# Performance work log

Hardware: AMD Instinct MI355X
Metric: run time of the kernel (lower is better)

## Reference

```python
import jax, jax.numpy as jnp
import numpy as np

TEMP = 1.0  # composition softmax temperature

def _bank_topk(x, U, V, logits, top_k):
    # softmax over primitive logits, select top-k, renormalize, fused low-rank projection
    w = jax.nn.softmax(logits / TEMP)                     # [P]
    tw, ti = jax.lax.top_k(w, top_k)                      # [k], [k]
    tw = tw / tw.sum()
    Us = U[ti]                                            # [k, d_in, r]
    Vs = V[ti]                                            # [k, r, d_out]
    h = jnp.einsum('bsd,kdr->bksr', x, Us)                # low-rank bottleneck
    return jnp.einsum('bksr,kro,k->bso', h, Vs, tw)       # weighted fuse

def reference(x, q_U, q_V, k_U, k_V, v_U, v_V, q_logits, k_logits, v_logits, out_w, top_k):
    B, S, _ = x.shape
    H, D = 16, 64
    q = _bank_topk(x, q_U, q_V, q_logits, top_k)
    k = _bank_topk(x, k_U, k_V, k_logits, top_k)
    v = _bank_topk(x, v_U, v_V, v_logits, top_k)
    q = q.reshape(B, S, H, D).transpose(0, 2, 1, 3)       # [B,H,S,D]
    k = k.reshape(B, S, H, D).transpose(0, 2, 1, 3)
    v = v.reshape(B, S, H, D).transpose(0, 2, 1, 3)
    scale = 1.0 / jnp.sqrt(jnp.asarray(D, dtype=x.dtype))
    scores = jnp.einsum('bhqd,bhkd->bhqk', q, k) * scale  # [B,H,S,S]
    causal = jnp.triu(jnp.ones((S, S), dtype=bool), 1)
    scores = jnp.where(causal[None, None], jnp.finfo(x.dtype).min, scores)
    probs = jax.nn.softmax(scores, axis=-1)
    out = jnp.einsum('bhqk,bhkd->bhqd', probs, v)
    out = out.transpose(0, 2, 1, 3).reshape(B, S, H * D)
    return out @ out_w.T                                   # nn.Linear(H*D, d_model, bias=False)

def setup_inputs() -> dict:
    key = jax.random.key(0)
    ks = jax.random.split(key, 11)
    P, d, r = 16, 1024, 64
    B, S = 4, 1024
    f = jnp.float32
    inp = {
        'x': jax.random.normal(ks[0], (B, S, d), f),
        'q_U': jax.random.normal(ks[1], (P, d, r), f) * (1.0 / np.sqrt(d)),
        'q_V': jax.random.normal(ks[2], (P, r, d), f) * (1.0 / np.sqrt(r)),
        'k_U': jax.random.normal(ks[3], (P, d, r), f) * (1.0 / np.sqrt(d)),
        'k_V': jax.random.normal(ks[4], (P, r, d), f) * (1.0 / np.sqrt(r)),
        'v_U': jax.random.normal(ks[5], (P, d, r), f) * (1.0 / np.sqrt(d)),
        'v_V': jax.random.normal(ks[6], (P, r, d), f) * (1.0 / np.sqrt(r)),
        'q_logits': jax.random.normal(ks[7], (P,), f) * 0.01,
        'k_logits': jax.random.normal(ks[8], (P,), f) * 0.01,
        'v_logits': jax.random.normal(ks[9], (P,), f) * 0.01,
        'out_w': jax.random.normal(ks[10], (d, d), f) * (1.0 / np.sqrt(d)),
        'top_k': 4,
    }
    return inp
```

## Files before the change

### kernel.cpp

```cpp
#include <hip/hip_runtime.h>
#include <math.h>

#define D_MODEL 1024
#define RANK    64
#define PMAX    16
#define S_LEN   1024
#define HD      64
#define MROWS   4096
#define NHEAD   16
#define BATCH   4

typedef short short8v __attribute__((ext_vector_type(8)));
typedef float floatx4 __attribute__((ext_vector_type(4)));

typedef __attribute__((address_space(1))) const unsigned int* gptr_t;
typedef __attribute__((address_space(3))) unsigned int* lptr_t;

static __device__ __forceinline__ void async16(const void* g, void* l) {
    __builtin_amdgcn_global_load_lds((gptr_t)g, (lptr_t)l, 16, 0, 0);
}

static __device__ __forceinline__ short f2bf(float f) {
    unsigned int u = __float_as_uint(f);
    u = (u + 0x7fffu + ((u >> 16) & 1u)) >> 16;
    return (short)u;
}

static __device__ __forceinline__ void topk_select(
    const float* __restrict__ lg, int K, int j, int* p_out, float* w_out) {
    float l[PMAX];
#pragma unroll
    for (int i = 0; i < PMAX; ++i) l[i] = lg[i];
    bool used[PMAX];
#pragma unroll
    for (int i = 0; i < PMAX; ++i) used[i] = false;
    float first = 0.f, sum = 0.f, sl = 0.f;
    int sel = 0;
    for (int jj = 0; jj < K; ++jj) {
        int best = -1; float bv = -INFINITY;
        for (int i = 0; i < PMAX; ++i)
            if (!used[i] && l[i] > bv) { bv = l[i]; best = i; }
        used[best] = true;
        if (jj == 0) first = bv;
        float e = __expf(bv - first);
        sum += e;
        if (jj == j) { sel = best; sl = e; }
    }
    if (j < K) { *p_out = sel; *w_out = sl / sum; }
    else       { *p_out = 0;   *w_out = 0.f; }
}

__global__ __launch_bounds__(256) void prep_all_kernel(
    const float* __restrict__ x,
    const float* __restrict__ qU, const float* __restrict__ kU,
    const float* __restrict__ vU,
    const float* __restrict__ qV, const float* __restrict__ kV,
    const float* __restrict__ vV,
    const float* __restrict__ qlg, const float* __restrict__ klg,
    const float* __restrict__ vlg,
    const int* __restrict__ topk, const float* __restrict__ outw,
    short* __restrict__ xb, short* __restrict__ wb,
    short* __restrict__ Ut, short* __restrict__ Vt) {
    int b = blockIdx.x;
    int t = threadIdx.x;
    if (b < 4096) {
        int i = b * 256 + t;
        float4 f = ((const float4*)x)[i];
        short4 o;
        o.x = f2bf(f.x); o.y = f2bf(f.y); o.z = f2bf(f.z); o.w = f2bf(f.w);
        ((short4*)xb)[i] = o;
        return;
    }
    if (b < 5120) {
        int i = (b - 4096) * 256 + t;
        float4 f = ((const float4*)outw)[i];
        short4 o;
        o.x = f2bf(f.x); o.y = f2bf(f.y); o.z = f2bf(f.z); o.w = f2bf(f.w);
        ((short4*)wb)[i] = o;
        return;
    }
    int rem  = b - 5120;
    int z    = rem >> 8;
    int j    = (rem >> 4) & 15;
    int tile = rem & 15;
    int bank = (z < 3) ? z : z - 3;
    int K = *topk; if (K < 1) K = 1; if (K > PMAX) K = PMAX;
    const float* lg = (bank == 0) ? qlg : (bank == 1) ? klg : vlg;
    int p; float wj;
    topk_select(lg, K, j, &p, &wj);

    __shared__ float T[64][65];
    if (z < 3) {
        const float* U = (bank == 0) ? qU : (bank == 1) ? kU : vU;
        const float* src = U + (size_t)p * D_MODEL * RANK;
        int d0 = tile * 64;
        int rl = t & 63, dq = t >> 6;
#pragma unroll
        for (int i = 0; i < 16; ++i) {
            int dl = i * 4 + dq;
            T[rl][dl] = src[(size_t)(d0 + dl) * RANK + rl];
        }
        __syncthreads();
        short* dst = Ut + (size_t)bank * D_MODEL * D_MODEL;
        int rr = t >> 2;
#pragma unroll
        for (int i = 0; i < 4; ++i) {
            int c = (t & 3) * 16 + i * 4;
            short4 o;
            o.x = f2bf(T[rr][c + 0]); o.y = f2bf(T[rr][c + 1]);
            o.z = f2bf(T[rr][c + 2]); o.w = f2bf(T[rr][c + 3]);
            *(short4*)&dst[(size_t)(j * 64 + rr) * D_MODEL + d0 + c] = o;
        }
    } else {
        const float* V = (bank == 0) ? qV : (bank == 1) ? kV : vV;
        const float* src = V + (size_t)p * RANK * D_MODEL;
        int n0 = tile * 64;
        int nl = t & 63, rq = t >> 6;
#pragma unroll
        for (int i = 0; i < 16; ++i) {
            int rl = i * 4 + rq;
            T[nl][rl] = src[(size_t)rl * D_MODEL + n0 + nl] * wj;
        }
        __syncthreads();
        short* dst = Vt + (size_t)bank * D_MODEL * D_MODEL;
        int rr = t >> 2;
#pragma unroll
        for (int i = 0; i < 4; ++i) {
            int c = (t & 3) * 16 + i * 4;
            short4 o;
            o.x = f2bf(T[rr][c + 0]); o.y = f2bf(T[rr][c + 1]);
            o.z = f2bf(T[rr][c + 2]); o.w = f2bf(T[rr][c + 3]);
            *(short4*)&dst[(size_t)(n0 + rr) * D_MODEL + j * 64 + c] = o;
        }
    }
}

static __device__ __forceinline__ void gemm_stage(
    const short* __restrict__ A, const short* __restrict__ B,
    int m0, int n0, int k0, short* Ab, short* Bb,
    int w, int srow, int skoff) {
    async16(A + (size_t)(m0 + w * 16 + srow) * D_MODEL + k0 + skoff,
            Ab + (w * 16 + srow) * 32 + skoff);
    async16(A + (size_t)(m0 + 64 + w * 16 + srow) * D_MODEL + k0 + skoff,
            Ab + (64 + w * 16 + srow) * 32 + skoff);
    async16(B + (size_t)(n0 + w * 16 + srow) * D_MODEL + k0 + skoff,
            Bb + (w * 16 + srow) * 32 + skoff);
    async16(B + (size_t)(n0 + 64 + w * 16 + srow) * D_MODEL + k0 + skoff,
            Bb + (64 + w * 16 + srow) * 32 + skoff);
}

static __device__ __forceinline__ void mfma_gemm_tile(
    const short* __restrict__ A, const short* __restrict__ B, int kl,
    int m0, int n0, short* As, short* Bs, floatx4 acc[4][4]) {
    const int t    = threadIdx.x;
    const int w    = t >> 6;
    const int lane = t & 63;
    const int wm   = w & 1, wn = w >> 1;
    const int colL = lane & 15, quad = lane >> 4;
    const int srow  = lane >> 2;
    const int skoff = (lane & 3) * 8;

#pragma unroll
    for (int i = 0; i < 4; ++i)
#pragma unroll
        for (int j = 0; j < 4; ++j) acc[i][j] = (floatx4){0.f, 0.f, 0.f, 0.f};

    gemm_stage(A, B, m0, n0, 0, As, Bs, w, srow, skoff);
    __syncthreads();
    const int nk = kl >> 5;
    int cur = 0;
    for (int kt = 0; kt < nk; ++kt) {
        if (kt + 1 < nk)
            gemm_stage(A, B, m0, n0, (kt + 1) * 32,
                       As + ((cur ^ 1) << 12), Bs + ((cur ^ 1) << 12),
                       w, srow, skoff);
        const short* Ab = As + (cur << 12);
        const short* Bb = Bs + (cur << 12);
        short8v af[4], bf[4];
#pragma unroll
        for (int i = 0; i < 4; ++i)
            af[i] = *(const short8v*)&Ab[(wm * 64 + i * 16 + colL) * 32 + quad * 8];
#pragma unroll
        for (int j = 0; j < 4; ++j)
            bf[j] = *(const short8v*)&Bb[(wn * 64 + j * 16 + colL) * 32 + quad * 8];
#pragma unroll
        for (int i = 0; i < 4; ++i)
#pragma unroll
            for (int j = 0; j < 4; ++j)
                acc[i][j] = __builtin_amdgcn_mfma_f32_16x16x32_bf16(af[i], bf[j], acc[i][j], 0, 0, 0);
        __syncthreads();
        cur ^= 1;
    }
}

__global__ __launch_bounds__(256) void gemm_h_kernel(
    const short* __restrict__ xb, const short* __restrict__ Ut,
    const int* __restrict__ topk, short* __restrict__ h) {
    int K = *topk; if (K < 1) K = 1; if (K > PMAX) K = PMAX;
    int n0 = blockIdx.y * 128;
    if (n0 >= K * 64) return;
    int m0 = blockIdx.x * 128;
    int bank = blockIdx.z;
    __shared__ short As[8192];
    __shared__ short Bs[8192];
    floatx4 acc[4][4];
    mfma_gemm_tile(xb, Ut + (size_t)bank * D_MODEL * D_MODEL, D_MODEL, m0, n0, As, Bs, acc);

    const int t = threadIdx.x, w = t >> 6, lane = t & 63;
    const int wm = w & 1, wn = w >> 1, colL = lane & 15, quad = lane >> 4;
    short* H = h + (size_t)bank * MROWS * D_MODEL;
#pragma unroll
    for (int i = 0; i < 4; ++i)
#pragma unroll
        for (int j = 0; j < 4; ++j)
#pragma unroll
            for (int r = 0; r < 4; ++r)
                H[(size_t)(m0 + wm * 64 + i * 16 + quad * 4 + r) * D_MODEL +
                  (n0 + wn * 64 + j * 16 + colL)] = f2bf(acc[i][j][r]);
}

__global__ __launch_bounds__(256) void gemm_qkv_kernel(
    const short* __restrict__ h, const short* __restrict__ Vt,
    const int* __restrict__ topk, short* __restrict__ qkv) {
    int K = *topk; if (K < 1) K = 1; if (K > PMAX) K = PMAX;
    int m0 = blockIdx.x * 128;
    int n0 = blockIdx.y * 128;
    int bank = blockIdx.z;
    __shared__ short As[8192];
    __shared__ short Bs[8192];
    floatx4 acc[4][4];
    mfma_gemm_tile(h + (size_t)bank * MROWS * D_MODEL,
                   Vt + (size_t)bank * D_MODEL * D_MODEL, K * 64, m0, n0, As, Bs, acc);

    const int t = threadIdx.x, w = t >> 6, lane = t & 63;
    const int wm = w & 1, wn = w >> 1, colL = lane & 15, quad = lane >> 4;
    short* outp = qkv + (size_t)bank * MROWS * D_MODEL;
    const float scl = (bank == 0) ? 0.18033688f : 1.0f;
#pragma unroll
    for (int i = 0; i < 4; ++i)
#pragma unroll
        for (int j = 0; j < 4; ++j)
#pragma unroll
            for (int r = 0; r < 4; ++r) {
                int m = m0 + wm * 64 + i * 16 + quad * 4 + r;
                int n = n0 + wn * 64 + j * 16 + colL;
                int b = m >> 10, s = m & 1023;
                int head = n >> 6, d = n & 63;
                outp[(((size_t)(b * NHEAD + head) << 10) + s) * HD + d] = f2bf(acc[i][j][r] * scl);
            }
}

__global__ __launch_bounds__(256) void transpose_v_kernel(
    const short* __restrict__ src, short* __restrict__ dst) {
    int st = blockIdx.x, bh = blockIdx.y;
    __shared__ short T[64][72];
    const short* S = src + (size_t)bh * (S_LEN * HD) + (size_t)st * 64 * HD;
    int r = threadIdx.x >> 2, i = threadIdx.x & 3;
    *(short8v*)&T[r][i * 16]     = *(const short8v*)&S[r * HD + i * 16];
    *(short8v*)&T[r][i * 16 + 8] = *(const short8v*)&S[r * HD + i * 16 + 8];
    __syncthreads();
    short* Drow = dst + (size_t)bh * (S_LEN * HD) + (size_t)r * S_LEN + st * 64 + i * 16;
    short8v o0, o1;
#pragma unroll
    for (int k = 0; k < 8; ++k) o0[k] = T[i * 16 + k][r];
#pragma unroll
    for (int k = 0; k < 8; ++k) o1[k] = T[i * 16 + 8 + k][r];
    *(short8v*)&Drow[0] = o0;
    *(short8v*)&Drow[8] = o1;
}

static __device__ __forceinline__ void attn_stage(
    const short* __restrict__ Kg, const short* __restrict__ Vg, int base,
    short* KsB, short* VsB, int w, int lane) {
#pragma unroll
    for (int q2 = 0; q2 < 4; ++q2) {
        int row = w * 32 + q2 * 8 + (lane >> 3);
        int i   = lane & 7;
        int g   = i ^ (row & 7);
        async16(Kg + (size_t)(base + row) * HD + g * 8, KsB + row * 64 + i * 8);
    }
#pragma unroll
    for (int q2 = 0; q2 < 4; ++q2) {
        int d    = w * 16 + q2 * 4 + (lane >> 4);
        int i    = lane & 15;
        int half = i >> 3, i3 = i & 7;
        int g3   = i3 ^ (d & 7);
        async16(Vg + (size_t)d * S_LEN + base + half * 64 + g3 * 8,
                VsB + d * 128 + i * 8);
    }
}

template<int NN, bool DIAG>
static __device__ __forceinline__ void attn_step(
    const short* KsB, const short* VsB, short* Pw,
    short8v aq0, short8v aq1, int w, int col, int quad,
    floatx4& O0, floatx4& O1, floatx4& O2, floatx4& O3,
    float mrow[4], float lrow[4]) {
    const int cl7 = col & 7;
    float sc[NN][4];
#pragma unroll
    for (int n = 0; n < NN; ++n) {
        const int dn = n - (NN - 4);
        if (DIAG && dn > w) {
#pragma unroll
            for (int r = 0; r < 4; ++r) sc[n][r] = -INFINITY;
        } else {
            floatx4 z = {0.f, 0.f, 0.f, 0.f};
            const short* kb = KsB + (n * 16 + col) * 64;
            short8v b0 = *(const short8v*)(kb + ((quad ^ cl7) << 3));
            short8v b1 = *(const short8v*)(kb + (((quad + 4) ^ cl7) << 3));
            z = __builtin_amdgcn_mfma_f32_16x16x32_bf16(aq0, b0, z, 0, 0, 0);
            z = __builtin_amdgcn_mfma_f32_16x16x32_bf16(aq1, b1, z, 0, 0, 0);
            if (DIAG && dn == w) {
#pragma unroll
                for (int r = 0; r < 4; ++r)
                    if (col > quad * 4 + r) z[r] = -INFINITY;
            }
#pragma unroll
            for (int r = 0; r < 4; ++r) sc[n][r] = z[r];
        }
    }
    float pv[NN][4];
#pragma unroll
    for (int r = 0; r < 4; ++r) {
        float tm = sc[0][r];
#pragma unroll
        for (int n = 1; n < NN; ++n) tm = fmaxf(tm, sc[n][r]);
        tm = fmaxf(tm, __shfl_xor(tm, 1));
        tm = fmaxf(tm, __shfl_xor(tm, 2));
        tm = fmaxf(tm, __shfl_xor(tm, 4));
        tm = fmaxf(tm, __shfl_xor(tm, 8));
        float mnew  = fmaxf(mrow[r], tm);
        float alpha = exp2f(mrow[r] - mnew);
        float ps = 0.f;
#pragma unroll
        for (int n = 0; n < NN; ++n) {
            float p = exp2f(sc[n][r] - mnew);
            pv[n][r] = p;
            ps += p;
        }
        lrow[r] = lrow[r] * alpha + ps;
        mrow[r] = mnew;
        O0[r] *= alpha; O1[r] *= alpha; O2[r] *= alpha; O3[r] *= alpha;
    }
#pragma unroll
    for (int h = 0; h < NN / 4; ++h) {
#pragma unroll
        for (int n2 = 0; n2 < 4; ++n2)
#pragma unroll
            for (int r = 0; r < 4; ++r)
                Pw[(quad * 4 + r) * 72 + n2 * 16 + col] = f2bf(pv[h * 4 + n2][r]);
        const int kslim = DIAG ? ((NN - 4 + w) >> 1) : 3;
#pragma unroll
        for (int ks2 = 2 * h; ks2 < 2 * h + 2; ++ks2) {
            if (DIAG && ks2 > kslim) break;
            short8v ap = *(const short8v*)(Pw + col * 72 + (ks2 & 1) * 32 + quad * 8);
            const int half = ks2 >> 1;
            const int i3   = (ks2 & 1) * 4 + quad;
            const int swz  = ((i3 ^ cl7) << 3);
            const short* vb = VsB + half * 64 + swz;
            short8v v0 = *(const short8v*)(vb + (0  + col) * 128);
            short8v v1 = *(const short8v*)(vb + (16 + col) * 128);
            short8v v2 = *(const short8v*)(vb + (32 + col) * 128);
            short8v v3 = *(const short8v*)(vb + (48 + col) * 128);
            O0 = __builtin_amdgcn_mfma_f32_16x16x32_bf16(ap, v0, O0, 0, 0, 0);
            O1 = __builtin_amdgcn_mfma_f32_16x16x32_bf16(ap, v1, O1, 0, 0, 0);
            O2 = __builtin_amdgcn_mfma_f32_16x16x32_bf16(ap, v2, O2, 0, 0, 0);
            O3 = __builtin_amdgcn_mfma_f32_16x16x32_bf16(ap, v3, O3, 0, 0, 0);
        }
    }
}

__global__ __launch_bounds__(256) void attn_mfma_kernel(
    const short* __restrict__ qkv,
    const short* __restrict__ vtb,
    short* __restrict__ attn_out) {
    const int t    = threadIdx.x;
    const int w    = t >> 6;
    const int lane = t & 63;
    const int col  = lane & 15;
    const int quad = lane >> 4;
    const int pr   = blockIdx.x;
    const int bh   = blockIdx.y;
    const size_t HS   = (size_t)S_LEN * HD;
    const size_t BSTR = (size_t)MROWS * D_MODEL;
    const short* Qg = qkv + (size_t)bh * HS;
    const short* Kg = qkv + BSTR + (size_t)bh * HS;
    const short* Vg = vtb + (size_t)bh * HS;

    __shared__ short Ks[2][8192];
    __shared__ short Vs[2][8192];
    __shared__ short Ps[4][1152];
    short* Pw = Ps[w];

    for (int ph = 0; ph < 2; ++ph) {
        const int qt = ph ? (15 - pr) : pr;
        const int qrow = qt * 64 + w * 16 + col;
        short8v aq0 = *(const short8v*)(Qg + (size_t)qrow * HD + quad * 8);
        short8v aq1 = *(const short8v*)(Qg + (size_t)qrow * HD + 32 + quad * 8);
        floatx4 O0 = {0.f, 0.f, 0.f, 0.f}, O1 = O0, O2 = O0, O3 = O0;
        float mrow[4] = {-INFINITY, -INFINITY, -INFINITY, -INFINITY};
        float lrow[4] = {0.f, 0.f, 0.f, 0.f};

        const int nC = (qt + 2) >> 1;
        __syncthreads();
        attn_stage(Kg, Vg, 0, Ks[0], Vs[0], w, lane);
        __syncthreads();
        int cur = 0;
        for (int c = 0; c + 1 < nC; ++c) {
            attn_stage(Kg, Vg, (c + 1) * 128, Ks[cur ^ 1], Vs[cur ^ 1], w, lane);
            attn_step<8, false>(Ks[cur], Vs[cur], Pw, aq0, aq1, w, col, quad,
                                O0, O1, O2, O3, mrow, lrow);
            __syncthreads();
            cur ^= 1;
        }
        if (qt & 1)
            attn_step<8, true>(Ks[cur], Vs[cur], Pw, aq0, aq1, w, col, quad,
                               O0, O1, O2, O3, mrow, lrow);
        else
            attn_step<4, true>(Ks[cur], Vs[cur], Pw, aq0, aq1, w, col, quad,
                               O0, O1, O2, O3, mrow, lrow);

        const int b  = bh >> 4;
        const int hh = bh & 15;
        short* orow = attn_out +
            ((size_t)(b * S_LEN) + qt * 64 + w * 16) * D_MODEL + hh * 64;
#pragma unroll
        for (int r = 0; r < 4; ++r) {
            float l = lrow[r];
            l += __shfl_xor(l, 1); l += __shfl_xor(l, 2);
            l += __shfl_xor(l, 4); l += __shfl_xor(l, 8);
            float inv = 1.f / l;
            short* prw = orow + (size_t)(quad * 4 + r) * D_MODEL;
            prw[0  + col] = f2bf(O0[r] * inv);
            prw[16 + col] = f2bf(O1[r] * inv);
            prw[32 + col] = f2bf(O2[r] * inv);
            prw[48 + col] = f2bf(O3[r] * inv);
        }
    }
}

__global__ __launch_bounds__(256) void gemm_proj_kernel(
    const short* __restrict__ attnb, const short* __restrict__ wb,
    float* __restrict__ outp) {
    int m0 = blockIdx.x * 128;
    int n0 = blockIdx.y * 128;
    __shared__ short As[8192];
    __shared__ short Bs[8192];
    floatx4 acc[4][4];
    mfma_gemm_tile(attnb, wb, D_MODEL, m0, n0, As, Bs, acc);

    const int t = threadIdx.x, w = t >> 6, lane = t & 63;
    const int wm = w & 1, wn = w >> 1, colL = lane & 15, quad = lane >> 4;
#pragma unroll
    for (int i = 0; i < 4; ++i)
#pragma unroll
        for (int j = 0; j < 4; ++j)
#pragma unroll
            for (int r = 0; r < 4; ++r)
                outp[(size_t)(m0 + wm * 64 + i * 16 + quad * 4 + r) * D_MODEL +
                     (n0 + wn * 64 + j * 16 + colL)] = acc[i][j][r];
}

extern "C" void kernel_launch(void* const* d_in, const int* in_sizes, int n_in,
                              void* d_out, int out_size, void* d_ws, size_t ws_size,
                              hipStream_t stream) {
    const float* x    = (const float*)d_in[0];
    const float* qU   = (const float*)d_in[1];
    const float* qV   = (const float*)d_in[2];
    const float* kU   = (const float*)d_in[3];
    const float* kV   = (const float*)d_in[4];
    const float* vU   = (const float*)d_in[5];
    const float* vV   = (const float*)d_in[6];
    const float* qlg  = (const float*)d_in[7];
    const float* klg  = (const float*)d_in[8];
    const float* vlg  = (const float*)d_in[9];
    const float* outw = (const float*)d_in[10];
    const int*   topk = (const int*)d_in[11];
    float* outp = (float*)d_out;

    char* ws = (char*)d_ws;
    short* xb   = (short*)ws;
    short* Ut   = xb + (size_t)MROWS * D_MODEL;
    short* Vt   = Ut + (size_t)3 * D_MODEL * D_MODEL;
    short* wb   = Vt + (size_t)3 * D_MODEL * D_MODEL;
    short* hbuf = wb + (size_t)D_MODEL * D_MODEL;
    short* qkvb = hbuf + (size_t)3 * MROWS * D_MODEL;
    short* attnb = qkvb + (size_t)3 * MROWS * D_MODEL;
    short* vtb  = attnb + (size_t)MROWS * D_MODEL;

    prep_all_kernel<<<6656, 256, 0, stream>>>(
        x, qU, kU, vU, qV, kV, vV, qlg, klg, vlg, topk, outw, xb, wb, Ut, Vt);
    gemm_h_kernel<<<dim3(32, 8, 3), 256, 0, stream>>>(xb, Ut, topk, hbuf);
    gemm_qkv_kernel<<<dim3(32, 8, 3), 256, 0, stream>>>(hbuf, Vt, topk, qkvb);
    transpose_v_kernel<<<dim3(16, 64), 256, 0, stream>>>(
        qkvb + (size_t)2 * MROWS * D_MODEL, vtb);
    attn_mfma_kernel<<<dim3(8, 64), 256, 0, stream>>>(qkvb, vtb, attnb);
    gemm_proj_kernel<<<dim3(32, 8), 256, 0, stream>>>(attnb, wb, outp);
}
```

Measured before the change: 252.6 us.

## Swap GEMM operands for vector stores and simplify attention to per-tile blocks

```diff
diff --git a/kernel.cpp b/kernel.cpp
--- a/kernel.cpp
+++ b/kernel.cpp
@@ -46,8 +46,7 @@
         sum += e;
         if (jj == j) { sel = best; sl = e; }
     }
-    if (j < K) { *p_out = sel; *w_out = sl / sum; }
-    else       { *p_out = 0;   *w_out = 0.f; }
+    *p_out = sel; *w_out = sl / sum;
 }
 
 __global__ __launch_bounds__(256) void prep_all_kernel(
@@ -85,6 +84,7 @@
     int tile = rem & 15;
     int bank = (z < 3) ? z : z - 3;
     int K = *topk; if (K < 1) K = 1; if (K > PMAX) K = PMAX;
+    if (j >= K) return;
     const float* lg = (bank == 0) ? qlg : (bank == 1) ? klg : vlg;
     int p; float wj;
     topk_select(lg, K, j, &p, &wj);
@@ -137,21 +137,21 @@
 
 static __device__ __forceinline__ void gemm_stage(
     const short* __restrict__ A, const short* __restrict__ B,
-    int m0, int n0, int k0, short* Ab, short* Bb,
+    int a0, int b0, int k0, short* Ab, short* Bb,
     int w, int srow, int skoff) {
-    async16(A + (size_t)(m0 + w * 16 + srow) * D_MODEL + k0 + skoff,
+    async16(A + (size_t)(a0 + w * 16 + srow) * D_MODEL + k0 + skoff,
             Ab + (w * 16 + srow) * 32 + skoff);
-    async16(A + (size_t)(m0 + 64 + w * 16 + srow) * D_MODEL + k0 + skoff,
+    async16(A + (size_t)(a0 + 64 + w * 16 + srow) * D_MODEL + k0 + skoff,
             Ab + (64 + w * 16 + srow) * 32 + skoff);
-    async16(B + (size_t)(n0 + w * 16 + srow) * D_MODEL + k0 + skoff,
+    async16(B + (size_t)(b0 + w * 16 + srow) * D_MODEL + k0 + skoff,
             Bb + (w * 16 + srow) * 32 + skoff);
-    async16(B + (size_t)(n0 + 64 + w * 16 + srow) * D_MODEL + k0 + skoff,
+    async16(B + (size_t)(b0 + 64 + w * 16 + srow) * D_MODEL + k0 + skoff,
             Bb + (64 + w * 16 + srow) * 32 + skoff);
 }
 
 static __device__ __forceinline__ void mfma_gemm_tile(
     const short* __restrict__ A, const short* __restrict__ B, int kl,
-    int m0, int n0, short* As, short* Bs, floatx4 acc[4][4]) {
+    int a0, int b0, short* As, short* Bs, floatx4 acc[4][4]) {
     const int t    = threadIdx.x;
     const int w    = t >> 6;
     const int lane = t & 63;
@@ -165,13 +165,13 @@
 #pragma unroll
         for (int j = 0; j < 4; ++j) acc[i][j] = (floatx4){0.f, 0.f, 0.f, 0.f};
 
-    gemm_stage(A, B, m0, n0, 0, As, Bs, w, srow, skoff);
+    gemm_stage(A, B, a0, b0, 0, As, Bs, w, srow, skoff);
     __syncthreads();
     const int nk = kl >> 5;
     int cur = 0;
     for (int kt = 0; kt < nk; ++kt) {
         if (kt + 1 < nk)
-            gemm_stage(A, B, m0, n0, (kt + 1) * 32,
+            gemm_stage(A, B, a0, b0, (kt + 1) * 32,
                        As + ((cur ^ 1) << 12), Bs + ((cur ^ 1) << 12),
                        w, srow, skoff);
         const short* Ab = As + (cur << 12);
@@ -204,7 +204,7 @@
     __shared__ short As[8192];
     __shared__ short Bs[8192];
     floatx4 acc[4][4];
-    mfma_gemm_tile(xb, Ut + (size_t)bank * D_MODEL * D_MODEL, D_MODEL, m0, n0, As, Bs, acc);
+    mfma_gemm_tile(Ut + (size_t)bank * D_MODEL * D_MODEL, xb, D_MODEL, n0, m0, As, Bs, acc);
 
     const int t = threadIdx.x, w = t >> 6, lane = t & 63;
     const int wm = w & 1, wn = w >> 1, colL = lane & 15, quad = lane >> 4;
@@ -212,11 +212,14 @@
 #pragma unroll
     for (int i = 0; i < 4; ++i)
 #pragma unroll
-        for (int j = 0; j < 4; ++j)
-#pragma unroll
-            for (int r = 0; r < 4; ++r)
-                H[(size_t)(m0 + wm * 64 + i * 16 + quad * 4 + r) * D_MODEL +
-                  (n0 + wn * 64 + j * 16 + colL)] = f2bf(acc[i][j][r]);
+        for (int j = 0; j < 4; ++j) {
+            int n = n0 + wm * 64 + i * 16 + quad * 4;
+            int m = m0 + wn * 64 + j * 16 + colL;
+            short4 o;
+            o.x = f2bf(acc[i][j][0]); o.y = f2bf(acc[i][j][1]);
+            o.z = f2bf(acc[i][j][2]); o.w = f2bf(acc[i][j][3]);
+            *(short4*)&H[(size_t)m * D_MODEL + n] = o;
+        }
 }
 
 __global__ __launch_bounds__(256) void gemm_qkv_kernel(
@@ -229,8 +232,8 @@
     __shared__ short As[8192];
     __shared__ short Bs[8192];
     floatx4 acc[4][4];
-    mfma_gemm_tile(h + (size_t)bank * MROWS * D_MODEL,
-                   Vt + (size_t)bank * D_MODEL * D_MODEL, K * 64, m0, n0, As, Bs, acc);
+    mfma_gemm_tile(Vt + (size_t)bank * D_MODEL * D_MODEL,
+                   h + (size_t)bank * MROWS * D_MODEL, K * 64, n0, m0, As, Bs, acc);
 
     const int t = threadIdx.x, w = t >> 6, lane = t & 63;
     const int wm = w & 1, wn = w >> 1, colL = lane & 15, quad = lane >> 4;
@@ -239,15 +242,16 @@
 #pragma unroll
     for (int i = 0; i < 4; ++i)
 #pragma unroll
-        for (int j = 0; j < 4; ++j)
-#pragma unroll
-            for (int r = 0; r < 4; ++r) {
-                int m = m0 + wm * 64 + i * 16 + quad * 4 + r;
-                int n = n0 + wn * 64 + j * 16 + colL;
-                int b = m >> 10, s = m & 1023;
-                int head = n >> 6, d = n & 63;
-                outp[(((size_t)(b * NHEAD + head) << 10) + s) * HD + d] = f2bf(acc[i][j][r] * scl);
-            }
+        for (int j = 0; j < 4; ++j) {
+            int n = n0 + wm * 64 + i * 16 + quad * 4;
+            int m = m0 + wn * 64 + j * 16 + colL;
+            int b = m >> 10, s = m & 1023;
+            int head = n >> 6, d = n & 63;
+            short4 o;
+            o.x = f2bf(acc[i][j][0] * scl); o.y = f2bf(acc[i][j][1] * scl);
+            o.z = f2bf(acc[i][j][2] * scl); o.w = f2bf(acc[i][j][3] * scl);
+            *(short4*)&outp[(((size_t)(b * NHEAD + head) << 10) + s) * HD + d] = o;
+        }
 }
 
 __global__ __launch_bounds__(256) void transpose_v_kernel(
@@ -269,105 +273,79 @@
     *(short8v*)&Drow[8] = o1;
 }
 
-static __device__ __forceinline__ void attn_stage(
-    const short* __restrict__ Kg, const short* __restrict__ Vg, int base,
+static __device__ __forceinline__ void stage_tiles(
+    const short* __restrict__ Kg, const short* __restrict__ Vg, int jt,
     short* KsB, short* VsB, int w, int lane) {
 #pragma unroll
-    for (int q2 = 0; q2 < 4; ++q2) {
-        int row = w * 32 + q2 * 8 + (lane >> 3);
-        int i   = lane & 7;
-        int g   = i ^ (row & 7);
-        async16(Kg + (size_t)(base + row) * HD + g * 8, KsB + row * 64 + i * 8);
-    }
-#pragma unroll
-    for (int q2 = 0; q2 < 4; ++q2) {
-        int d    = w * 16 + q2 * 4 + (lane >> 4);
-        int i    = lane & 15;
-        int half = i >> 3, i3 = i & 7;
-        int g3   = i3 ^ (d & 7);
-        async16(Vg + (size_t)d * S_LEN + base + half * 64 + g3 * 8,
-                VsB + d * 128 + i * 8);
-    }
-}
-
-template<int NN, bool DIAG>
+    for (int q = 0; q < 2; ++q) {
+        int c   = q * 64 + lane;
+        int r16 = c >> 3;
+        int i   = c & 7;
+        int r   = w * 16 + r16;
+        int g   = i ^ (r16 & 7);
+        async16(Kg + (size_t)(jt * 64 + r) * HD + g * 8, KsB + r * 64 + i * 8);
+        async16(Vg + (size_t)r * S_LEN + jt * 64 + g * 8, VsB + r * 64 + i * 8);
+    }
+}
+
+template<bool DIAG>
 static __device__ __forceinline__ void attn_step(
     const short* KsB, const short* VsB, short* Pw,
     short8v aq0, short8v aq1, int w, int col, int quad,
     floatx4& O0, floatx4& O1, floatx4& O2, floatx4& O3,
     float mrow[4], float lrow[4]) {
     const int cl7 = col & 7;
-    float sc[NN][4];
-#pragma unroll
-    for (int n = 0; n < NN; ++n) {
-        const int dn = n - (NN - 4);
-        if (DIAG && dn > w) {
-#pragma unroll
-            for (int r = 0; r < 4; ++r) sc[n][r] = -INFINITY;
-        } else {
+    floatx4 c4[4];
+#pragma unroll
+    for (int n = 0; n < 4; ++n) {
+        if (!DIAG || n <= w) {
             floatx4 z = {0.f, 0.f, 0.f, 0.f};
-            const short* kb = KsB + (n * 16 + col) * 64;
-            short8v b0 = *(const short8v*)(kb + ((quad ^ cl7) << 3));
-            short8v b1 = *(const short8v*)(kb + (((quad + 4) ^ cl7) << 3));
+            short8v b0 = *(const short8v*)&KsB[(n * 16 + col) * 64 + ((quad ^ cl7) << 3)];
+            short8v b1 = *(const short8v*)&KsB[(n * 16 + col) * 64 + (((quad + 4) ^ cl7) << 3)];
             z = __builtin_amdgcn_mfma_f32_16x16x32_bf16(aq0, b0, z, 0, 0, 0);
             z = __builtin_amdgcn_mfma_f32_16x16x32_bf16(aq1, b1, z, 0, 0, 0);
-            if (DIAG && dn == w) {
+            if (DIAG) {
 #pragma unroll
                 for (int r = 0; r < 4; ++r)
-                    if (col > quad * 4 + r) z[r] = -INFINITY;
+                    if (n == w && col > quad * 4 + r) z[r] = -INFINITY;
             }
-#pragma unroll
-            for (int r = 0; r < 4; ++r) sc[n][r] = z[r];
-        }
-    }
-    float pv[NN][4];
+            c4[n] = z;
+        } else {
+            c4[n] = (floatx4){-INFINITY, -INFINITY, -INFINITY, -INFINITY};
+        }
+    }
 #pragma unroll
     for (int r = 0; r < 4; ++r) {
-        float tm = sc[0][r];
-#pragma unroll
-        for (int n = 1; n < NN; ++n) tm = fmaxf(tm, sc[n][r]);
+        float tm = fmaxf(fmaxf(c4[0][r], c4[1][r]), fmaxf(c4[2][r], c4[3][r]));
         tm = fmaxf(tm, __shfl_xor(tm, 1));
         tm = fmaxf(tm, __shfl_xor(tm, 2));
         tm = fmaxf(tm, __shfl_xor(tm, 4));
         tm = fmaxf(tm, __shfl_xor(tm, 8));
         float mnew  = fmaxf(mrow[r], tm);
         float alpha = exp2f(mrow[r] - mnew);
-        float ps = 0.f;
-#pragma unroll
-        for (int n = 0; n < NN; ++n) {
-            float p = exp2f(sc[n][r] - mnew);
-            pv[n][r] = p;
-            ps += p;
-        }
-        lrow[r] = lrow[r] * alpha + ps;
+        float p0 = exp2f(c4[0][r] - mnew), p1 = exp2f(c4[1][r] - mnew);
+        float p2 = exp2f(c4[2][r] - mnew), p3 = exp2f(c4[3][r] - mnew);
+        lrow[r] = lrow[r] * alpha + (p0 + p1 + p2 + p3);
         mrow[r] = mnew;
         O0[r] *= alpha; O1[r] *= alpha; O2[r] *= alpha; O3[r] *= alpha;
-    }
-#pragma unroll
-    for (int h = 0; h < NN / 4; ++h) {
-#pragma unroll
-        for (int n2 = 0; n2 < 4; ++n2)
-#pragma unroll
-            for (int r = 0; r < 4; ++r)
-                Pw[(quad * 4 + r) * 72 + n2 * 16 + col] = f2bf(pv[h * 4 + n2][r]);
-        const int kslim = DIAG ? ((NN - 4 + w) >> 1) : 3;
-#pragma unroll
-        for (int ks2 = 2 * h; ks2 < 2 * h + 2; ++ks2) {
-            if (DIAG && ks2 > kslim) break;
-            short8v ap = *(const short8v*)(Pw + col * 72 + (ks2 & 1) * 32 + quad * 8);
-            const int half = ks2 >> 1;
-            const int i3   = (ks2 & 1) * 4 + quad;
-            const int swz  = ((i3 ^ cl7) << 3);
-            const short* vb = VsB + half * 64 + swz;
-            short8v v0 = *(const short8v*)(vb + (0  + col) * 128);
-            short8v v1 = *(const short8v*)(vb + (16 + col) * 128);
-            short8v v2 = *(const short8v*)(vb + (32 + col) * 128);
-            short8v v3 = *(const short8v*)(vb + (48 + col) * 128);
-            O0 = __builtin_amdgcn_mfma_f32_16x16x32_bf16(ap, v0, O0, 0, 0, 0);
-            O1 = __builtin_amdgcn_mfma_f32_16x16x32_bf16(ap, v1, O1, 0, 0, 0);
-            O2 = __builtin_amdgcn_mfma_f32_16x16x32_bf16(ap, v2, O2, 0, 0, 0);
-            O3 = __builtin_amdgcn_mfma_f32_16x16x32_bf16(ap, v3, O3, 0, 0, 0);
-        }
+        short* pr = Pw + (quad * 4 + r) * 72 + col;
+        pr[0]  = f2bf(p0); pr[16] = f2bf(p1);
+        pr[32] = f2bf(p2); pr[48] = f2bf(p3);
+    }
+    const int ksmax = DIAG ? (w >> 1) : 1;
+#pragma unroll
+    for (int ks = 0; ks < 2; ++ks) {
+        if (ks > ksmax) break;
+        short8v ap = *(const short8v*)&Pw[col * 72 + ks * 32 + quad * 8];
+        int pc = ((ks * 4 + quad) ^ cl7) << 3;
+        short8v v0 = *(const short8v*)&VsB[(0  + col) * 64 + pc];
+        short8v v1 = *(const short8v*)&VsB[(16 + col) * 64 + pc];
+        short8v v2 = *(const short8v*)&VsB[(32 + col) * 64 + pc];
+        short8v v3 = *(const short8v*)&VsB[(48 + col) * 64 + pc];
+        O0 = __builtin_amdgcn_mfma_f32_16x16x32_bf16(ap, v0, O0, 0, 0, 0);
+        O1 = __builtin_amdgcn_mfma_f32_16x16x32_bf16(ap, v1, O1, 0, 0, 0);
+        O2 = __builtin_amdgcn_mfma_f32_16x16x32_bf16(ap, v2, O2, 0, 0, 0);
+        O3 = __builtin_amdgcn_mfma_f32_16x16x32_bf16(ap, v3, O3, 0, 0, 0);
     }
 }
 
@@ -380,7 +358,7 @@
     const int lane = t & 63;
     const int col  = lane & 15;
     const int quad = lane >> 4;
-    const int pr   = blockIdx.x;
+    const int qt   = blockIdx.x;
     const int bh   = blockIdx.y;
     const size_t HS   = (size_t)S_LEN * HD;
     const size_t BSTR = (size_t)MROWS * D_MODEL;
@@ -388,55 +366,45 @@
     const short* Kg = qkv + BSTR + (size_t)bh * HS;
     const short* Vg = vtb + (size_t)bh * HS;
 
-    __shared__ short Ks[2][8192];
-    __shared__ short Vs[2][8192];
+    __shared__ short Ks[4096];
+    __shared__ short Vs[4096];
     __shared__ short Ps[4][1152];
     short* Pw = Ps[w];
 
-    for (int ph = 0; ph < 2; ++ph) {
-        const int qt = ph ? (15 - pr) : pr;
-        const int qrow = qt * 64 + w * 16 + col;
-        short8v aq0 = *(const short8v*)(Qg + (size_t)qrow * HD + quad * 8);
-        short8v aq1 = *(const short8v*)(Qg + (size_t)qrow * HD + 32 + quad * 8);
-        floatx4 O0 = {0.f, 0.f, 0.f, 0.f}, O1 = O0, O2 = O0, O3 = O0;
-        float mrow[4] = {-INFINITY, -INFINITY, -INFINITY, -INFINITY};
-        float lrow[4] = {0.f, 0.f, 0.f, 0.f};
-
-        const int nC = (qt + 2) >> 1;
+    const int qrow = qt * 64 + w * 16 + col;
+    short8v aq0 = *(const short8v*)(Qg + (size_t)qrow * HD + quad * 8);
+    short8v aq1 = *(const short8v*)(Qg + (size_t)qrow * HD + 32 + quad * 8);
+    floatx4 O0 = {0.f, 0.f, 0.f, 0.f}, O1 = O0, O2 = O0, O3 = O0;
+    float mrow[4] = {-INFINITY, -INFINITY, -INFINITY, -INFINITY};
+    float lrow[4] = {0.f, 0.f, 0.f, 0.f};
+
+    for (int jt = 0; jt <= qt; ++jt) {
         __syncthreads();
-        attn_stage(Kg, Vg, 0, Ks[0], Vs[0], w, lane);
+        stage_tiles(Kg, Vg, jt, Ks, Vs, w, lane);
         __syncthreads();
-        int cur = 0;
-        for (int c = 0; c + 1 < nC; ++c) {
-            attn_stage(Kg, Vg, (c + 1) * 128, Ks[cur ^ 1], Vs[cur ^ 1], w, lane);
-            attn_step<8, false>(Ks[cur], Vs[cur], Pw, aq0, aq1, w, col, quad,
-                                O0, O1, O2, O3, mrow, lrow);
-            __syncthreads();
-            cur ^= 1;
-        }
-        if (qt & 1)
-            attn_step<8, true>(Ks[cur], Vs[cur], Pw, aq0, aq1, w, col, quad,
-                               O0, O1, O2, O3, mrow, lrow);
+        if (jt < qt)
+            attn_step<false>(Ks, Vs, Pw, aq0, aq1, w, col, quad,
+                             O0, O1, O2, O3, mrow, lrow);
         else
-            attn_step<4, true>(Ks[cur], Vs[cur], Pw, aq0, aq1, w, col, quad,
-                               O0, O1, O2, O3, mrow, lrow);
-
-        const int b  = bh >> 4;
-        const int hh = bh & 15;
-        short* orow = attn_out +
-            ((size_t)(b * S_LEN) + qt * 64 + w * 16) * D_MODEL + hh * 64;
-#pragma unroll
-        for (int r = 0; r < 4; ++r) {
-            float l = lrow[r];
-            l += __shfl_xor(l, 1); l += __shfl_xor(l, 2);
-            l += __shfl_xor(l, 4); l += __shfl_xor(l, 8);
-            float inv = 1.f / l;
-            short* prw = orow + (size_t)(quad * 4 + r) * D_MODEL;
-            prw[0  + col] = f2bf(O0[r] * inv);
-            prw[16 + col] = f2bf(O1[r] * inv);
-            prw[32 + col] = f2bf(O2[r] * inv);
-            prw[48 + col] = f2bf(O3[r] * inv);
-        }
+            attn_step<true>(Ks, Vs, Pw, aq0, aq1, w, col, quad,
+                            O0, O1, O2, O3, mrow, lrow);
+    }
+
+    const int b  = bh >> 4;
+    const int hh = bh & 15;
+    short* orow = attn_out +
+        ((size_t)(b * S_LEN) + qt * 64 + w * 16) * D_MODEL + hh * 64;
+#pragma unroll
+    for (int r = 0; r < 4; ++r) {
+        float l = lrow[r];
+        l += __shfl_xor(l, 1); l += __shfl_xor(l, 2);
+        l += __shfl_xor(l, 4); l += __shfl_xor(l, 8);
+        float inv = 1.f / l;
+        short* prw = orow + (size_t)(quad * 4 + r) * D_MODEL;
+        prw[0  + col] = f2bf(O0[r] * inv);
+        prw[16 + col] = f2bf(O1[r] * inv);
+        prw[32 + col] = f2bf(O2[r] * inv);
+        prw[48 + col] = f2bf(O3[r] * inv);
     }
 }
 
@@ -448,18 +416,20 @@
     __shared__ short As[8192];
     __shared__ short Bs[8192];
     floatx4 acc[4][4];
-    mfma_gemm_tile(attnb, wb, D_MODEL, m0, n0, As, Bs, acc);
+    mfma_gemm_tile(wb, attnb, D_MODEL, n0, m0, As, Bs, acc);
 
     const int t = threadIdx.x, w = t >> 6, lane = t & 63;
     const int wm = w & 1, wn = w >> 1, colL = lane & 15, quad = lane >> 4;
 #pragma unroll
     for (int i = 0; i < 4; ++i)
 #pragma unroll
-        for (int j = 0; j < 4; ++j)
-#pragma unroll
-            for (int r = 0; r < 4; ++r)
-                outp[(size_t)(m0 + wm * 64 + i * 16 + quad * 4 + r) * D_MODEL +
-                     (n0 + wn * 64 + j * 16 + colL)] = acc[i][j][r];
+        for (int j = 0; j < 4; ++j) {
+            int n = n0 + wm * 64 + i * 16 + quad * 4;
+            int m = m0 + wn * 64 + j * 16 + colL;
+            float4 o = make_float4(acc[i][j][0], acc[i][j][1],
+                                   acc[i][j][2], acc[i][j][3]);
+            *(float4*)&outp[(size_t)m * D_MODEL + n] = o;
+        }
 }
 
 extern "C" void kernel_launch(void* const* d_in, const int* in_sizes, int n_in,
@@ -495,6 +465,6 @@
     gemm_qkv_kernel<<<dim3(32, 8, 3), 256, 0, stream>>>(hbuf, Vt, topk, qkvb);
     transpose_v_kernel<<<dim3(16, 64), 256, 0, stream>>>(
         qkvb + (size_t)2 * MROWS * D_MODEL, vtb);
-    attn_mfma_kernel<<<dim3(8, 64), 256, 0, stream>>>(qkvb, vtb, attnb);
+    attn_mfma_kernel<<<dim3(16, 64), 256, 0, stream>>>(qkvb, vtb, attnb);
     gemm_proj_kernel<<<dim3(32, 8), 256, 0, stream>>>(attnb, wb, outp);
 }
```

Result: slower. 274.4 us (+8.6%).
